# Performance work log

Measured on AMD Instinct MI355X. Metric: run time of the kernel, lower is better.

The kernel has to match this reference:

```python
import jax, jax.numpy as jnp
import numpy as np

S, H, A = 16384, 1024, 1024


def setup_inputs() -> dict:
    key = jax.random.key(0)
    k1, k2, k3, k4, k5, k6 = jax.random.split(key, 6)
    enc_out = jax.random.normal(k1, (S, 1, H), dtype=jnp.float32)
    dec_h = jax.random.normal(k2, (1, H), dtype=jnp.float32)
    mask = jax.random.randint(k3, (S, 1), 0, 2) == 1  # bool [S,1]
    # learned params (torch Linear stores weight as [out, in]; y = x @ W.T)
    W2_dec = jax.random.normal(k4, (A, H), dtype=jnp.float32) * 0.02
    W1_enc = jax.random.normal(k5, (A, H), dtype=jnp.float32) * 0.02
    V = jax.random.normal(k6, (1, A), dtype=jnp.float32) * 0.02
    return {"enc_out": enc_out, "dec_h": dec_h, "mask": mask,
            "W2_dec": W2_dec, "W1_enc": W1_enc, "V": V}


def reference(enc_out, dec_h, mask, W2_dec, W1_enc, V):
    enc = jnp.squeeze(enc_out, axis=1)            # [S, H]
    d = dec_h @ W2_dec.T                          # [1, A]
    e = enc @ W1_enc.T                            # [S, A]
    u = jnp.tanh(d + e) @ V.T                     # [S, 1]
    u = jnp.where(mask, -jnp.inf, u)              # masked logits (returned, like in-place fill)
    a = jax.nn.softmax(u, axis=0)                 # softmax over seq dim
    out = jnp.sum(a * enc, axis=0)                # [H]
    return (out, u)
```

## Files before the change

### kernel.cpp

```cpp
#include <hip/hip_runtime.h>
#include <math.h>
#include <stdint.h>

#define S_DIM 16384
#define H_DIM 1024
#define A_DIM 1024

#define MASK_NEG (-3.0e38f)

typedef __attribute__((ext_vector_type(8))) _Float16 f16x8;
typedef __attribute__((ext_vector_type(4))) float f32x4;
typedef __attribute__((address_space(3))) uint32_t as3_u32;
typedef __attribute__((address_space(1))) uint32_t as1_u32;

__global__ __launch_bounds__(256) void prep_kernel(
        const float* __restrict__ enc, _Float16* __restrict__ enc_h,
        const float* __restrict__ W1, _Float16* __restrict__ W1_h,
        const float* __restrict__ dec_h, const float* __restrict__ W2,
        float* __restrict__ d, float* __restrict__ u_acc) {
    const int b = blockIdx.x;
    const int t = threadIdx.x;
    if (b < 8704) {
        const float* src = (b < 8192) ? enc : W1;
        _Float16* dst    = (b < 8192) ? enc_h : W1_h;
        const int i = ((b < 8192) ? b : (b - 8192)) * 256 + t;
        float4 v0 = ((const float4*)src)[2 * i];
        float4 v1 = ((const float4*)src)[2 * i + 1];
        union { _Float16 h[8]; uint4 u; } pk;
        pk.h[0] = (_Float16)v0.x; pk.h[1] = (_Float16)v0.y;
        pk.h[2] = (_Float16)v0.z; pk.h[3] = (_Float16)v0.w;
        pk.h[4] = (_Float16)v1.x; pk.h[5] = (_Float16)v1.y;
        pk.h[6] = (_Float16)v1.z; pk.h[7] = (_Float16)v1.w;
        ((uint4*)dst)[i] = pk.u;
        if (b < 64) u_acc[b * 256 + t] = 0.0f;
    } else {
        const int a = b - 8704;
        const float* row = W2 + (size_t)a * H_DIM;
        float s = 0.0f;
        for (int h = t; h < H_DIM; h += 256) s += dec_h[h] * row[h];
        #pragma unroll
        for (int off = 32; off; off >>= 1) s += __shfl_down(s, off, 64);
        __shared__ float wsum[4];
        if ((t & 63) == 0) wsum[t >> 6] = s;
        __syncthreads();
        if (t == 0) d[a] = wsum[0] + wsum[1] + wsum[2] + wsum[3];
    }
}

__global__ __launch_bounds__(512, 1) void fused_gemm_f16_2ph(
        const _Float16* __restrict__ Ag,
        const _Float16* __restrict__ Bg,
        const float* __restrict__ V,
        const float* __restrict__ d,
        float* __restrict__ u_acc) {
    __shared__ __align__(16) _Float16 AB[2][32768];

    const int tid  = threadIdx.x;
    const int wave = tid >> 6;
    const int lane = tid & 63;
    const int quad = lane >> 4;
    const int l16  = lane & 15;
    const int wm   = wave >> 2;
    const int wn   = wave & 3;
    const int s0   = blockIdx.x * 256;
    const int a0   = blockIdx.y * 256;

    const _Float16* gsrc = (wave < 4) ? Ag : Bg;
    const int rbase      = (wave < 4) ? s0 : a0;
    const int rowoff     = (wave & 3) * 64;
    const int lrow = lane >> 2;
    const int cg   = ((lane & 3) + (lrow >> 1)) & 3;

    const _Float16* grow[4];
    #pragma unroll
    for (int j = 0; j < 4; ++j)
        grow[j] = gsrc + (size_t)(rbase + rowoff + j * 16 + lrow) * H_DIM + cg * 8;
    _Float16* lbase0 = &AB[0][((wave < 4) ? 0 : 8192) + rowoff * 32];

    const int sw = ((quad - (l16 >> 1)) & 3) * 8;
    int aoff[8], boff[4];
    #pragma unroll
    for (int mi = 0; mi < 8; ++mi)
        aoff[mi] = (wm * 128 + mi * 16 + l16) * 32 + sw;
    #pragma unroll
    for (int ni = 0; ni < 4; ++ni)
        boff[ni] = 8192 + (wn * 64 + ni * 16 + l16) * 32 + sw;

    f32x4 acc[8][4];
    #pragma unroll
    for (int mi = 0; mi < 8; ++mi)
        #pragma unroll
        for (int ni = 0; ni < 4; ++ni)
            acc[mi][ni] = (f32x4){0.f, 0.f, 0.f, 0.f};

    const _Float16* hAB = &AB[0][0];

    #pragma unroll
    for (int s = 0; s < 2; ++s)
        #pragma unroll
        for (int j = 0; j < 4; ++j)
            __builtin_amdgcn_global_load_lds(
                (const as1_u32*)(const void*)(grow[j] + s * 32),
                (as3_u32*)(void*)(lbase0 + s * 16384 + j * 512), 16, 0, 0);
    __syncthreads();

    for (int ph = 0; ph < 16; ++ph) {
        const int b = ph & 1;
        if (ph < 15) {
            #pragma unroll
            for (int s = 0; s < 2; ++s)
                #pragma unroll
                for (int j = 0; j < 4; ++j)
                    __builtin_amdgcn_global_load_lds(
                        (const as1_u32*)(const void*)(grow[j] + ((ph + 1) * 2 + s) * 32),
                        (as3_u32*)(void*)(lbase0 + (b ^ 1) * 32768 + s * 16384 + j * 512),
                        16, 0, 0);
        }
        #pragma unroll
        for (int s = 0; s < 2; ++s) {
            const int base = b * 32768 + s * 16384;
            f16x8 bf[4];
            #pragma unroll
            for (int ni = 0; ni < 4; ++ni)
                bf[ni] = *(const f16x8*)&hAB[base + boff[ni]];
            #pragma unroll
            for (int mi = 0; mi < 8; ++mi) {
                f16x8 af = *(const f16x8*)&hAB[base + aoff[mi]];
                #pragma unroll
                for (int ni = 0; ni < 4; ++ni)
                    acc[mi][ni] = __builtin_amdgcn_mfma_f32_16x16x32_f16(af, bf[ni], acc[mi][ni], 0, 0, 0);
            }
        }
        __syncthreads();
    }

    float* P = (float*)&AB[0][0];
    float vv[4], dd[4];
    #pragma unroll
    for (int ni = 0; ni < 4; ++ni) {
        int c = a0 + wn * 64 + ni * 16 + l16;
        vv[ni] = V[c];
        dd[ni] = d[c];
    }
    #pragma unroll
    for (int mi = 0; mi < 8; ++mi) {
        #pragma unroll
        for (int reg = 0; reg < 4; ++reg) {
            float s = 0.0f;
            #pragma unroll
            for (int ni = 0; ni < 4; ++ni)
                s += vv[ni] * tanhf(dd[ni] + acc[mi][ni][reg]);
            #pragma unroll
            for (int off = 1; off < 16; off <<= 1)
                s += __shfl_xor(s, off, 64);
            if (l16 == 0)
                P[(wm * 128 + mi * 16 + quad * 4 + reg) * 4 + wn] = s;
        }
    }
    __syncthreads();
    if (tid < 256)
        atomicAdd(u_acc + s0 + tid,
                  P[tid * 4 + 0] + P[tid * 4 + 1] + P[tid * 4 + 2] + P[tid * 4 + 3]);
}

__global__ __launch_bounds__(512, 2) void fused_gemm_f16(
        const _Float16* __restrict__ Ag, const _Float16* __restrict__ Bg,
        const float* __restrict__ V, const float* __restrict__ d,
        float* __restrict__ u_acc) {
    __shared__ __align__(16) _Float16 AB[2][16384];

    const int tid  = threadIdx.x;
    const int wave = tid >> 6;
    const int lane = tid & 63;
    const int quad = lane >> 4;
    const int l16  = lane & 15;
    const int wm   = wave >> 2;
    const int wn   = wave & 3;
    const int s0   = blockIdx.x * 256;
    const int a0   = blockIdx.y * 256;

    const _Float16* gsrc = (wave < 4) ? Ag : Bg;
    const int rbase      = (wave < 4) ? s0 : a0;
    const int rowoff     = (wave & 3) * 64;
    const int lrow = lane >> 2;
    const int cg   = ((lane & 3) + (lrow >> 1)) & 3;

    const _Float16* grow[4];
    #pragma unroll
    for (int j = 0; j < 4; ++j)
        grow[j] = gsrc + (size_t)(rbase + rowoff + j * 16 + lrow) * H_DIM + cg * 8;
    _Float16* lbase0 = &AB[0][((wave < 4) ? 0 : 8192) + rowoff * 32];

    const int sw = ((quad - (l16 >> 1)) & 3) * 8;
    int aoff[8], boff[4];
    #pragma unroll
    for (int mi = 0; mi < 8; ++mi)
        aoff[mi] = (wm * 128 + mi * 16 + l16) * 32 + sw;
    #pragma unroll
    for (int ni = 0; ni < 4; ++ni)
        boff[ni] = 8192 + (wn * 64 + ni * 16 + l16) * 32 + sw;

    f32x4 acc[8][4];
    #pragma unroll
    for (int mi = 0; mi < 8; ++mi)
        #pragma unroll
        for (int ni = 0; ni < 4; ++ni)
            acc[mi][ni] = (f32x4){0.f, 0.f, 0.f, 0.f};

    #pragma unroll
    for (int j = 0; j < 4; ++j)
        __builtin_amdgcn_global_load_lds(
            (const as1_u32*)(const void*)(grow[j]),
            (as3_u32*)(void*)(lbase0 + j * 512), 16, 0, 0);
    __syncthreads();

    for (int kt = 0; kt < H_DIM / 32; kt += 2) {
        {
            #pragma unroll
            for (int j = 0; j < 4; ++j)
                __builtin_amdgcn_global_load_lds(
                    (const as1_u32*)(const void*)(grow[j] + (kt + 1) * 32),
                    (as3_u32*)(void*)(lbase0 + 16384 + j * 512), 16, 0, 0);
        }
        {
            f16x8 bf[4];
            #pragma unroll
            for (int ni = 0; ni < 4; ++ni) bf[ni] = *(const f16x8*)&AB[0][boff[ni]];
            #pragma unroll
            for (int mi = 0; mi < 8; ++mi) {
                f16x8 af = *(const f16x8*)&AB[0][aoff[mi]];
                #pragma unroll
                for (int ni = 0; ni < 4; ++ni)
                    acc[mi][ni] = __builtin_amdgcn_mfma_f32_16x16x32_f16(af, bf[ni], acc[mi][ni], 0, 0, 0);
            }
        }
        __syncthreads();
        if (kt + 2 < H_DIM / 32) {
            #pragma unroll
            for (int j = 0; j < 4; ++j)
                __builtin_amdgcn_global_load_lds(
                    (const as1_u32*)(const void*)(grow[j] + (kt + 2) * 32),
                    (as3_u32*)(void*)(lbase0 + j * 512), 16, 0, 0);
        }
        {
            f16x8 bf[4];
            #pragma unroll
            for (int ni = 0; ni < 4; ++ni) bf[ni] = *(const f16x8*)&AB[1][boff[ni]];
            #pragma unroll
            for (int mi = 0; mi < 8; ++mi) {
                f16x8 af = *(const f16x8*)&AB[1][aoff[mi]];
                #pragma unroll
                for (int ni = 0; ni < 4; ++ni)
                    acc[mi][ni] = __builtin_amdgcn_mfma_f32_16x16x32_f16(af, bf[ni], acc[mi][ni], 0, 0, 0);
            }
        }
        __syncthreads();
    }

    float* P = (float*)&AB[0][0];
    float vv[4], dd[4];
    #pragma unroll
    for (int ni = 0; ni < 4; ++ni) {
        int c = a0 + wn * 64 + ni * 16 + l16;
        vv[ni] = V[c];
        dd[ni] = d[c];
    }
    #pragma unroll
    for (int mi = 0; mi < 8; ++mi) {
        #pragma unroll
        for (int reg = 0; reg < 4; ++reg) {
            float s = 0.0f;
            #pragma unroll
            for (int ni = 0; ni < 4; ++ni)
                s += vv[ni] * tanhf(dd[ni] + acc[mi][ni][reg]);
            #pragma unroll
            for (int off = 1; off < 16; off <<= 1)
                s += __shfl_xor(s, off, 64);
            if (l16 == 0)
                P[(wm * 128 + mi * 16 + quad * 4 + reg) * 4 + wn] = s;
        }
    }
    __syncthreads();
    if (tid < 256)
        atomicAdd(u_acc + s0 + tid,
                  P[tid * 4 + 0] + P[tid * 4 + 1] + P[tid * 4 + 2] + P[tid * 4 + 3]);
}

__global__ __launch_bounds__(256) void fused_gemm(const float* __restrict__ enc,
                                                  const float* __restrict__ W1,
                                                  const float* __restrict__ V,
                                                  const float* __restrict__ d,
                                                  float* __restrict__ u_acc) {
    __shared__ __align__(16) float As[16][128 + 4];
    __shared__ __align__(16) float Bs[16][128 + 4];
    const int tid = threadIdx.x;
    const int tx = tid & 15, ty = tid >> 4;
    const int s0 = blockIdx.y * 128, a0 = blockIdx.x * 128;
    const int lr = tid >> 2, lc = tid & 3;
    float acc[8][8] = {};
    for (int kt = 0; kt < H_DIM / 16; ++kt) {
        const int k0 = kt * 16;
        float4 av0 = *(const float4*)(enc + (size_t)(s0 + lr)      * H_DIM + k0 + 4 * lc);
        float4 av1 = *(const float4*)(enc + (size_t)(s0 + lr + 64) * H_DIM + k0 + 4 * lc);
        float4 bv0 = *(const float4*)(W1  + (size_t)(a0 + lr)      * H_DIM + k0 + 4 * lc);
        float4 bv1 = *(const float4*)(W1  + (size_t)(a0 + lr + 64) * H_DIM + k0 + 4 * lc);
        __syncthreads();
        As[4*lc+0][lr] = av0.x; As[4*lc+1][lr] = av0.y; As[4*lc+2][lr] = av0.z; As[4*lc+3][lr] = av0.w;
        As[4*lc+0][lr+64] = av1.x; As[4*lc+1][lr+64] = av1.y; As[4*lc+2][lr+64] = av1.z; As[4*lc+3][lr+64] = av1.w;
        Bs[4*lc+0][lr] = bv0.x; Bs[4*lc+1][lr] = bv0.y; Bs[4*lc+2][lr] = bv0.z; Bs[4*lc+3][lr] = bv0.w;
        Bs[4*lc+0][lr+64] = bv1.x; Bs[4*lc+1][lr+64] = bv1.y; Bs[4*lc+2][lr+64] = bv1.z; Bs[4*lc+3][lr+64] = bv1.w;
        __syncthreads();
        #pragma unroll
        for (int k = 0; k < 16; ++k) {
            float4 A0 = *(const float4*)&As[k][8 * ty];
            float4 A1 = *(const float4*)&As[k][8 * ty + 4];
            float4 B0 = *(const float4*)&Bs[k][8 * tx];
            float4 B1 = *(const float4*)&Bs[k][8 * tx + 4];
            float ar[8] = {A0.x, A0.y, A0.z, A0.w, A1.x, A1.y, A1.z, A1.w};
            float br[8] = {B0.x, B0.y, B0.z, B0.w, B1.x, B1.y, B1.z, B1.w};
            #pragma unroll
            for (int i = 0; i < 8; ++i)
                #pragma unroll
                for (int j = 0; j < 8; ++j)
                    acc[i][j] = fmaf(ar[i], br[j], acc[i][j]);
        }
    }
    float vv[8], dd[8];
    #pragma unroll
    for (int j = 0; j < 8; ++j) { int c = a0 + 8 * tx + j; vv[j] = V[c]; dd[j] = d[c]; }
    float pu[8];
    #pragma unroll
    for (int i = 0; i < 8; ++i) {
        float s = 0.0f;
        #pragma unroll
        for (int j = 0; j < 8; ++j) s += vv[j] * tanhf(dd[j] + acc[i][j]);
        pu[i] = s;
    }
    __syncthreads();
    float* Pf = &As[0][0];
    #pragma unroll
    for (int i = 0; i < 8; ++i) Pf[(8 * ty + i) * 16 + tx] = pu[i];
    __syncthreads();
    if (tid < 128) {
        float s = 0.0f;
        #pragma unroll
        for (int j = 0; j < 16; ++j) s += Pf[tid * 16 + j];
        atomicAdd(u_acc + s0 + tid, s);
    }
}

__global__ __launch_bounds__(1024) void softmax_kernel(const float* __restrict__ u_acc,
                                                       const void* __restrict__ mask,
                                                       float* __restrict__ u_out,
                                                       float* __restrict__ p) {
    const int t = threadIdx.x;
    const unsigned char* mb = (const unsigned char*)mask;
    const int* mi = (const int*)mask;

    unsigned int orv = 0;
    for (int i = t; i < S_DIM; i += 1024)
        if (i & 3) orv |= mb[i];
    __shared__ int sflag;
    if (t == 0) sflag = 0;
    __syncthreads();
    if (orv) sflag = 1;
    __syncthreads();
    const int bytemask = sflag;

    float v[16];
    float lmax = -INFINITY;
    #pragma unroll
    for (int i = 0; i < 16; ++i) {
        int r = t + i * 1024;
        int m = bytemask ? (int)mb[r] : mi[r];
        float val = m ? MASK_NEG : u_acc[r];
        u_out[r] = val;
        v[i] = val;
        lmax = fmaxf(lmax, val);
    }

    __shared__ float red[16];
    __shared__ float sm, sdenom;
    #pragma unroll
    for (int off = 32; off; off >>= 1) lmax = fmaxf(lmax, __shfl_down(lmax, off, 64));
    int wid = t >> 6, lane = t & 63;
    if (lane == 0) red[wid] = lmax;
    __syncthreads();
    if (t == 0) {
        float m2 = -INFINITY;
        for (int i = 0; i < 16; ++i) m2 = fmaxf(m2, red[i]);
        sm = m2;
    }
    __syncthreads();
    const float m = sm;

    float lsum = 0.0f;
    #pragma unroll
    for (int i = 0; i < 16; ++i) {
        v[i] = expf(v[i] - m);
        lsum += v[i];
    }
    #pragma unroll
    for (int off = 32; off; off >>= 1) lsum += __shfl_down(lsum, off, 64);
    if (lane == 0) red[wid] = lsum;
    __syncthreads();
    if (t == 0) {
        float s2 = 0.0f;
        for (int i = 0; i < 16; ++i) s2 += red[i];
        sdenom = s2;
    }
    __syncthreads();
    const float inv = 1.0f / sdenom;
    #pragma unroll
    for (int i = 0; i < 16; ++i) p[t + i * 1024] = v[i] * inv;
}

__global__ __launch_bounds__(256) void wsum_part(const _Float16* __restrict__ enc_h,
                                                 const float* __restrict__ p,
                                                 float* __restrict__ part) {
    const int t = threadIdx.x;
    const int b = blockIdx.x;
    float4 acc = {0.f, 0.f, 0.f, 0.f};
    const int s0 = b * 32;
    for (int s = s0; s < s0 + 32; ++s) {
        float ps = p[s];
        union { _Float16 h[4]; uint2 u; } e;
        e.u = ((const uint2*)(enc_h + (size_t)s * H_DIM))[t];
        acc.x += ps * (float)e.h[0];
        acc.y += ps * (float)e.h[1];
        acc.z += ps * (float)e.h[2];
        acc.w += ps * (float)e.h[3];
    }
    ((float4*)(part + (size_t)b * 1024))[t] = acc;
}
__global__ __launch_bounds__(256) void wsum_reduce(const float* __restrict__ part,
                                                   float* __restrict__ out) {
    __shared__ float red[256];
    const int t = threadIdx.x;
    const int col = blockIdx.x * 16 + (t & 15);
    const int seg = t >> 4;
    float s = 0.0f;
    for (int b = seg * 32; b < seg * 32 + 32; ++b)
        s += part[(size_t)b * 1024 + col];
    red[t] = s;
    __syncthreads();
    if (t < 16) {
        float r = 0.0f;
        #pragma unroll
        for (int k = 0; k < 16; ++k) r += red[k * 16 + t];
        out[col] = r;
    }
}
__global__ __launch_bounds__(256) void weighted_sum(const float* __restrict__ enc,
                                                    const float* __restrict__ p,
                                                    float* __restrict__ out) {
    const int t = threadIdx.x;
    const int s0 = blockIdx.x * 32;
    const float4* encv = (const float4*)enc;
    float4 acc = {0.0f, 0.0f, 0.0f, 0.0f};
    for (int s = s0; s < s0 + 32; ++s) {
        float ps = p[s];
        float4 e = encv[(size_t)s * 256 + t];
        acc.x += ps * e.x; acc.y += ps * e.y; acc.z += ps * e.z; acc.w += ps * e.w;
    }
    atomicAdd(out + 4 * t + 0, acc.x);
    atomicAdd(out + 4 * t + 1, acc.y);
    atomicAdd(out + 4 * t + 2, acc.z);
    atomicAdd(out + 4 * t + 3, acc.w);
}
__global__ void zero_kernel(float* __restrict__ u_acc, float* __restrict__ out) {
    int i = blockIdx.x * 256 + threadIdx.x;
    if (i < S_DIM) u_acc[i] = 0.0f;
    if (i < H_DIM) out[i]   = 0.0f;
}
__global__ __launch_bounds__(256) void dec_proj(const float* __restrict__ dec_h,
                                                const float* __restrict__ W2,
                                                float* __restrict__ d) {
    int a = blockIdx.x;
    int t = threadIdx.x;
    const float* row = W2 + (size_t)a * H_DIM;
    float s = 0.0f;
    for (int h = t; h < H_DIM; h += 256) s += dec_h[h] * row[h];
    #pragma unroll
    for (int off = 32; off; off >>= 1) s += __shfl_down(s, off, 64);
    __shared__ float wsum[4];
    if ((t & 63) == 0) wsum[t >> 6] = s;
    __syncthreads();
    if (t == 0) d[a] = wsum[0] + wsum[1] + wsum[2] + wsum[3];
}

extern "C" void kernel_launch(void* const* d_in, const int* in_sizes, int n_in,
                              void* d_out, int out_size, void* d_ws, size_t ws_size,
                              hipStream_t stream) {
    const float* enc   = (const float*)d_in[0];
    const float* dec_h = (const float*)d_in[1];
    const void*  mask  = d_in[2];
    const float* W2    = (const float*)d_in[3];
    const float* W1    = (const float*)d_in[4];
    const float* V     = (const float*)d_in[5];

    float* out   = (float*)d_out;
    float* u_out = (float*)d_out + H_DIM;

    float* ws    = (float*)d_ws;
    float* d     = ws;
    float* u_acc = ws + A_DIM;
    float* p     = ws + A_DIM + S_DIM;
    float* part  = ws + A_DIM + 2 * S_DIM;
    size_t f_end = (size_t)(A_DIM + 2 * S_DIM + 512 * 1024);
    _Float16* enc_h = (_Float16*)(ws + f_end);
    _Float16* W1_h  = enc_h + (size_t)S_DIM * H_DIM;
    size_t need_bytes = f_end * 4
                      + (size_t)S_DIM * H_DIM * 2
                      + (size_t)A_DIM * H_DIM * 2;

    int dev = 0;
    hipGetDevice(&dev);
    int max_lds = 0;
    hipDeviceGetAttribute(&max_lds, hipDeviceAttributeMaxSharedMemoryPerBlock, dev);

    if (ws_size >= need_bytes) {
        prep_kernel<<<9728, 256, 0, stream>>>(enc, enc_h, W1, W1_h,
                                              dec_h, W2, d, u_acc);
        if (max_lds >= 131072) {
            fused_gemm_f16_2ph<<<dim3(S_DIM / 256, A_DIM / 256), 512, 0, stream>>>(
                enc_h, W1_h, V, d, u_acc);
        } else {
            fused_gemm_f16<<<dim3(S_DIM / 256, A_DIM / 256), 512, 0, stream>>>(
                enc_h, W1_h, V, d, u_acc);
        }
        softmax_kernel<<<1, 1024, 0, stream>>>(u_acc, mask, u_out, p);
        wsum_part<<<S_DIM / 32, 256, 0, stream>>>(enc_h, p, part);
        wsum_reduce<<<64, 256, 0, stream>>>(part, out);
    } else {
        zero_kernel<<<64, 256, 0, stream>>>(u_acc, out);
        dec_proj<<<A_DIM, 256, 0, stream>>>(dec_h, W2, d);
        fused_gemm<<<dim3(A_DIM / 128, S_DIM / 128), 256, 0, stream>>>(enc, W1, V, d, u_acc);
        softmax_kernel<<<1, 1024, 0, stream>>>(u_acc, mask, u_out, p);
        weighted_sum<<<S_DIM / 32, 256, 0, stream>>>(enc, p, out);
    }
}
```

Before: 185.3 us.

## Add warp-specialized producer-consumer GEMM with four-stage LDS ring buffer

Introduces a 768-thread GEMM kernel with four dedicated producer waves. They stream fp16 tiles into a four-deep LDS ring through global_load_lds and signal readiness with LDS counters. Eight consumer waves spin on those flags and run the MFMA loop without block-wide barriers. The aim is deeper copy/compute overlap and fewer __syncthreads stalls. The cost is spin-waiting, extra waves per CU and reliance on correct vmcnt ordering. The old 512-thread fallback is removed and replaced by the fp32 path.

```diff
diff --git a/kernel.cpp b/kernel.cpp
--- a/kernel.cpp
+++ b/kernel.cpp
@@ -12,6 +12,9 @@
 typedef __attribute__((ext_vector_type(4))) float f32x4;
 typedef __attribute__((address_space(3))) uint32_t as3_u32;
 typedef __attribute__((address_space(1))) uint32_t as1_u32;
+
+#define WAITCNT_VM8 0x0F78
+#define WAITCNT_VM0 0x0F70
 
 __global__ __launch_bounds__(256) void prep_kernel(
         const float* __restrict__ enc, _Float16* __restrict__ enc_h,
@@ -47,11 +50,141 @@
     }
 }
 
-__global__ __launch_bounds__(512, 1) void fused_gemm_f16_2ph(
+__global__ __launch_bounds__(768) void fused_gemm_f16_pc(
         const _Float16* __restrict__ Ag,
         const _Float16* __restrict__ Bg,
         const float* __restrict__ V,
         const float* __restrict__ d,
+        float* __restrict__ u_acc) {
+    __shared__ __align__(16) _Float16 AB[4][16384];
+    __shared__ float P[256][4];
+    __shared__ unsigned ready_f[64];
+    __shared__ unsigned done_f[64];
+
+    const int tid  = threadIdx.x;
+    const int wave = tid >> 6;
+    const int lane = tid & 63;
+    const int quad = lane >> 4;
+    const int l16  = lane & 15;
+    const int s0   = blockIdx.x * 256;
+    const int a0   = blockIdx.y * 256;
+
+    if (tid < 64) { ready_f[tid] = 0u; done_f[tid] = 0u; }
+    __syncthreads();
+
+    if (wave >= 8) {
+        const int p    = wave - 8;
+        const int lrow = lane >> 2;
+        const int cg   = ((lane & 3) + (lrow >> 1)) & 3;
+        const _Float16* gsrc = (p < 2) ? Ag : Bg;
+        const int rbase = (p < 2) ? s0 : a0;
+        const int rloc  = (p & 1) * 128;
+        const _Float16* grow[8];
+        #pragma unroll
+        for (int j = 0; j < 8; ++j)
+            grow[j] = gsrc + (size_t)(rbase + rloc + j * 16 + lrow) * H_DIM + cg * 8;
+        const int ldst = ((p < 2) ? 0 : 8192) + rloc * 32;
+
+        #pragma unroll
+        for (int j = 0; j < 8; ++j)
+            __builtin_amdgcn_global_load_lds(
+                (const as1_u32*)(const void*)(grow[j]),
+                (as3_u32*)(void*)(&AB[0][ldst + j * 512]), 16, 0, 0);
+
+        for (int c = 0; c < 64; ++c) {
+            if (c < 63) {
+                const int fr = c - 3;
+                if (fr >= 0)
+                    while (*(volatile unsigned*)&done_f[fr] < 8u)
+                        __builtin_amdgcn_s_sleep(2);
+                __builtin_amdgcn_sched_barrier(0);
+                #pragma unroll
+                for (int j = 0; j < 8; ++j)
+                    __builtin_amdgcn_global_load_lds(
+                        (const as1_u32*)(const void*)(grow[j] + (c + 1) * 32),
+                        (as3_u32*)(void*)(&AB[(c + 1) & 3][ldst + j * 512]), 16, 0, 0);
+                __builtin_amdgcn_sched_barrier(0);
+                __builtin_amdgcn_s_waitcnt(WAITCNT_VM8);
+            } else {
+                __builtin_amdgcn_sched_barrier(0);
+                __builtin_amdgcn_s_waitcnt(WAITCNT_VM0);
+            }
+            __builtin_amdgcn_sched_barrier(0);
+            if (lane == 0) atomicAdd(&ready_f[c], 1u);
+        }
+    } else {
+        const int wm = wave >> 2;
+        const int wn = wave & 3;
+        const int sw = ((quad - (l16 >> 1)) & 3) * 8;
+        int aoff[8], boff[4];
+        #pragma unroll
+        for (int mi = 0; mi < 8; ++mi)
+            aoff[mi] = (wm * 128 + mi * 16 + l16) * 32 + sw;
+        #pragma unroll
+        for (int ni = 0; ni < 4; ++ni)
+            boff[ni] = 8192 + (wn * 64 + ni * 16 + l16) * 32 + sw;
+
+        f32x4 acc[8][4];
+        #pragma unroll
+        for (int mi = 0; mi < 8; ++mi)
+            #pragma unroll
+            for (int ni = 0; ni < 4; ++ni)
+                acc[mi][ni] = (f32x4){0.f, 0.f, 0.f, 0.f};
+
+        for (int c = 0; c < 64; ++c) {
+            while (*(volatile unsigned*)&ready_f[c] < 4u)
+                __builtin_amdgcn_s_sleep(2);
+            __builtin_amdgcn_sched_barrier(0);
+            const _Float16* base = &AB[c & 3][0];
+            f16x8 bf[4];
+            #pragma unroll
+            for (int ni = 0; ni < 4; ++ni)
+                bf[ni] = *(const f16x8*)&base[boff[ni]];
+            #pragma unroll
+            for (int mi = 0; mi < 8; ++mi) {
+                f16x8 af = *(const f16x8*)&base[aoff[mi]];
+                #pragma unroll
+                for (int ni = 0; ni < 4; ++ni)
+                    acc[mi][ni] = __builtin_amdgcn_mfma_f32_16x16x32_f16(
+                        af, bf[ni], acc[mi][ni], 0, 0, 0);
+            }
+            __builtin_amdgcn_sched_barrier(0);
+            if (lane == 0) atomicAdd(&done_f[c], 1u);
+        }
+
+        float vv[4], dd[4];
+        #pragma unroll
+        for (int ni = 0; ni < 4; ++ni) {
+            int cc = a0 + wn * 64 + ni * 16 + l16;
+            vv[ni] = V[cc];
+            dd[ni] = d[cc];
+        }
+        #pragma unroll
+        for (int mi = 0; mi < 8; ++mi) {
+            #pragma unroll
+            for (int reg = 0; reg < 4; ++reg) {
+                float s = 0.0f;
+                #pragma unroll
+                for (int ni = 0; ni < 4; ++ni)
+                    s += vv[ni] * tanhf(dd[ni] + acc[mi][ni][reg]);
+                #pragma unroll
+                for (int off = 1; off < 16; off <<= 1)
+                    s += __shfl_xor(s, off, 64);
+                if (l16 == 0)
+                    P[wm * 128 + mi * 16 + quad * 4 + reg][wn] = s;
+            }
+        }
+    }
+
+    __syncthreads();
+    if (tid < 256)
+        atomicAdd(u_acc + s0 + tid,
+                  P[tid][0] + P[tid][1] + P[tid][2] + P[tid][3]);
+}
+
+__global__ __launch_bounds__(512, 1) void fused_gemm_f16_2ph(
+        const _Float16* __restrict__ Ag, const _Float16* __restrict__ Bg,
+        const float* __restrict__ V, const float* __restrict__ d,
         float* __restrict__ u_acc) {
     __shared__ __align__(16) _Float16 AB[2][32768];
 
@@ -94,7 +227,6 @@
             acc[mi][ni] = (f32x4){0.f, 0.f, 0.f, 0.f};
 
     const _Float16* hAB = &AB[0][0];
-
     #pragma unroll
     for (int s = 0; s < 2; ++s)
         #pragma unroll
@@ -126,129 +258,6 @@
             #pragma unroll
             for (int mi = 0; mi < 8; ++mi) {
                 f16x8 af = *(const f16x8*)&hAB[base + aoff[mi]];
-                #pragma unroll
-                for (int ni = 0; ni < 4; ++ni)
-                    acc[mi][ni] = __builtin_amdgcn_mfma_f32_16x16x32_f16(af, bf[ni], acc[mi][ni], 0, 0, 0);
-            }
-        }
-        __syncthreads();
-    }
-
-    float* P = (float*)&AB[0][0];
-    float vv[4], dd[4];
-    #pragma unroll
-    for (int ni = 0; ni < 4; ++ni) {
-        int c = a0 + wn * 64 + ni * 16 + l16;
-        vv[ni] = V[c];
-        dd[ni] = d[c];
-    }
-    #pragma unroll
-    for (int mi = 0; mi < 8; ++mi) {
-        #pragma unroll
-        for (int reg = 0; reg < 4; ++reg) {
-            float s = 0.0f;
-            #pragma unroll
-            for (int ni = 0; ni < 4; ++ni)
-                s += vv[ni] * tanhf(dd[ni] + acc[mi][ni][reg]);
-            #pragma unroll
-            for (int off = 1; off < 16; off <<= 1)
-                s += __shfl_xor(s, off, 64);
-            if (l16 == 0)
-                P[(wm * 128 + mi * 16 + quad * 4 + reg) * 4 + wn] = s;
-        }
-    }
-    __syncthreads();
-    if (tid < 256)
-        atomicAdd(u_acc + s0 + tid,
-                  P[tid * 4 + 0] + P[tid * 4 + 1] + P[tid * 4 + 2] + P[tid * 4 + 3]);
-}
-
-__global__ __launch_bounds__(512, 2) void fused_gemm_f16(
-        const _Float16* __restrict__ Ag, const _Float16* __restrict__ Bg,
-        const float* __restrict__ V, const float* __restrict__ d,
-        float* __restrict__ u_acc) {
-    __shared__ __align__(16) _Float16 AB[2][16384];
-
-    const int tid  = threadIdx.x;
-    const int wave = tid >> 6;
-    const int lane = tid & 63;
-    const int quad = lane >> 4;
-    const int l16  = lane & 15;
-    const int wm   = wave >> 2;
-    const int wn   = wave & 3;
-    const int s0   = blockIdx.x * 256;
-    const int a0   = blockIdx.y * 256;
-
-    const _Float16* gsrc = (wave < 4) ? Ag : Bg;
-    const int rbase      = (wave < 4) ? s0 : a0;
-    const int rowoff     = (wave & 3) * 64;
-    const int lrow = lane >> 2;
-    const int cg   = ((lane & 3) + (lrow >> 1)) & 3;
-
-    const _Float16* grow[4];
-    #pragma unroll
-    for (int j = 0; j < 4; ++j)
-        grow[j] = gsrc + (size_t)(rbase + rowoff + j * 16 + lrow) * H_DIM + cg * 8;
-    _Float16* lbase0 = &AB[0][((wave < 4) ? 0 : 8192) + rowoff * 32];
-
-    const int sw = ((quad - (l16 >> 1)) & 3) * 8;
-    int aoff[8], boff[4];
-    #pragma unroll
-    for (int mi = 0; mi < 8; ++mi)
-        aoff[mi] = (wm * 128 + mi * 16 + l16) * 32 + sw;
-    #pragma unroll
-    for (int ni = 0; ni < 4; ++ni)
-        boff[ni] = 8192 + (wn * 64 + ni * 16 + l16) * 32 + sw;
-
-    f32x4 acc[8][4];
-    #pragma unroll
-    for (int mi = 0; mi < 8; ++mi)
-        #pragma unroll
-        for (int ni = 0; ni < 4; ++ni)
-            acc[mi][ni] = (f32x4){0.f, 0.f, 0.f, 0.f};
-
-    #pragma unroll
-    for (int j = 0; j < 4; ++j)
-        __builtin_amdgcn_global_load_lds(
-            (const as1_u32*)(const void*)(grow[j]),
-            (as3_u32*)(void*)(lbase0 + j * 512), 16, 0, 0);
-    __syncthreads();
-
-    for (int kt = 0; kt < H_DIM / 32; kt += 2) {
-        {
-            #pragma unroll
-            for (int j = 0; j < 4; ++j)
-                __builtin_amdgcn_global_load_lds(
-                    (const as1_u32*)(const void*)(grow[j] + (kt + 1) * 32),
-                    (as3_u32*)(void*)(lbase0 + 16384 + j * 512), 16, 0, 0);
-        }
-        {
-            f16x8 bf[4];
-            #pragma unroll
-            for (int ni = 0; ni < 4; ++ni) bf[ni] = *(const f16x8*)&AB[0][boff[ni]];
-            #pragma unroll
-            for (int mi = 0; mi < 8; ++mi) {
-                f16x8 af = *(const f16x8*)&AB[0][aoff[mi]];
-                #pragma unroll
-                for (int ni = 0; ni < 4; ++ni)
-                    acc[mi][ni] = __builtin_amdgcn_mfma_f32_16x16x32_f16(af, bf[ni], acc[mi][ni], 0, 0, 0);
-            }
-        }
-        __syncthreads();
-        if (kt + 2 < H_DIM / 32) {
-            #pragma unroll
-            for (int j = 0; j < 4; ++j)
-                __builtin_amdgcn_global_load_lds(
-                    (const as1_u32*)(const void*)(grow[j] + (kt + 2) * 32),
-                    (as3_u32*)(void*)(lbase0 + j * 512), 16, 0, 0);
-        }
-        {
-            f16x8 bf[4];
-            #pragma unroll
-            for (int ni = 0; ni < 4; ++ni) bf[ni] = *(const f16x8*)&AB[1][boff[ni]];
-            #pragma unroll
-            for (int mi = 0; mi < 8; ++mi) {
-                f16x8 af = *(const f16x8*)&AB[1][aoff[mi]];
                 #pragma unroll
                 for (int ni = 0; ni < 4; ++ni)
                     acc[mi][ni] = __builtin_amdgcn_mfma_f32_16x16x32_f16(af, bf[ni], acc[mi][ni], 0, 0, 0);
@@ -522,12 +531,15 @@
     if (ws_size >= need_bytes) {
         prep_kernel<<<9728, 256, 0, stream>>>(enc, enc_h, W1, W1_h,
                                               dec_h, W2, d, u_acc);
-        if (max_lds >= 131072) {
+        if (max_lds >= 135680) {
+            fused_gemm_f16_pc<<<dim3(S_DIM / 256, A_DIM / 256), 768, 0, stream>>>(
+                enc_h, W1_h, V, d, u_acc);
+        } else if (max_lds >= 131072) {
             fused_gemm_f16_2ph<<<dim3(S_DIM / 256, A_DIM / 256), 512, 0, stream>>>(
                 enc_h, W1_h, V, d, u_acc);
         } else {
-            fused_gemm_f16<<<dim3(S_DIM / 256, A_DIM / 256), 512, 0, stream>>>(
-                enc_h, W1_h, V, d, u_acc);
+            zero_kernel<<<64, 256, 0, stream>>>(u_acc, out);
+            fused_gemm<<<dim3(A_DIM / 128, S_DIM / 128), 256, 0, stream>>>(enc, W1, V, d, u_acc);
         }
         softmax_kernel<<<1, 1024, 0, stream>>>(u_acc, mask, u_out, p);
         wsum_part<<<S_DIM / 32, 256, 0, stream>>>(enc_h, p, part);
```

Result: slower. 215.5 us (+16.3%).
